# Kernel optimization log

Hardware: AMD Instinct MI355X
Metric: run time of the kernel (lower is better)

## Reference

```python
import math
import jax, jax.numpy as jnp
import numpy as np

B, S, D = 64, 729, 64  # S = (32*14//16 - 1)**2

def setup_inputs() -> dict:
    key = jax.random.key(0)
    kq, kk, kv, km = jax.random.split(key, 4)
    return {
        "query": jax.random.normal(kq, (B, S, D), dtype=jnp.float32),
        "key": jax.random.normal(kk, (B, S, D), dtype=jnp.float32),
        "value": jax.random.normal(kv, (B, S, D), dtype=jnp.float32),
        "mask": jax.random.randint(km, (B, S, S), 0, 2, dtype=jnp.int32),
    }

def reference(query, key, value, mask):
    dk = query.shape[-1]
    # [B,S,S] scores
    scores = jnp.einsum('bqd,bkd->bqk', query, key) / math.sqrt(dk)
    scores = jnp.where(mask == 0, jnp.float32(-1e9), scores)
    attention = jnp.tanh(scores)  # args.activation == 'tanh'
    # ignore_diag == 1: zero the diagonal of each [S,S] attention map
    eye = jnp.eye(attention.shape[-1], dtype=attention.dtype)
    attention = attention * (1.0 - eye)
    out = jnp.einsum('bqk,bkd->bqd', attention, value)
    return (out, attention)
```

## Files before the change

kernel.cpp:

```cpp
#include <hip/hip_runtime.h>

#define BATCH 64
#define SEQ 729
#define DIM 64
#define NT 12
#define STRB 72
#define MSTR 68
#define OSTR 68

typedef __attribute__((ext_vector_type(8))) short bf16x8;
typedef __attribute__((ext_vector_type(4))) float f32x4;
typedef int   i32x4a __attribute__((ext_vector_type(4), aligned(4)));
typedef float f32x4a __attribute__((ext_vector_type(4), aligned(4)));

__device__ __forceinline__ unsigned short f2bf(float f) {
    unsigned int u = __float_as_uint(f);
    u += 0x7fffu + ((u >> 16) & 1u);
    return (unsigned short)(u >> 16);
}

__device__ __forceinline__ unsigned long long pack4bf(float a, float b, float c, float d) {
    return (unsigned long long)f2bf(a)
         | ((unsigned long long)f2bf(b) << 16)
         | ((unsigned long long)f2bf(c) << 32)
         | ((unsigned long long)f2bf(d) << 48);
}

__device__ __forceinline__ float bf2f(unsigned int hi16) {
    return __uint_as_float(hi16 << 16);
}

__device__ __forceinline__ float fast_tanh(float x) {
    float e = __builtin_amdgcn_exp2f(x * 2.88539008177792681f);
    return 1.0f - 2.0f * __builtin_amdgcn_rcpf(e + 1.0f);
}

#define BAR() do { \
    asm volatile("s_waitcnt lgkmcnt(0)" ::: "memory"); \
    __builtin_amdgcn_s_barrier(); \
    __builtin_amdgcn_sched_barrier(0); \
} while (0)

__global__ __launch_bounds__(256, 3) void attn_kernel(
    const float* __restrict__ Qg, const float* __restrict__ Kg,
    const float* __restrict__ Vg, const int* __restrict__ Mg,
    float* __restrict__ Og, float* __restrict__ Ag)
{
    __shared__ __align__(16) unsigned char smem[50432];
    unsigned short* Ks0 = (unsigned short*)(smem);
    unsigned short* Vs0 = (unsigned short*)(smem + 9216);
    unsigned short* Ks1 = (unsigned short*)(smem + 18432);
    unsigned short* Vs1 = (unsigned short*)(smem + 27648);
    unsigned short* Ps  = (unsigned short*)(smem + 36864);
    unsigned char*  Mb8 = smem + 46080;
    float* Ostage = (float*)smem;

    const int tid = threadIdx.x;
    const int q0  = blockIdx.x * 64;
    const int b   = blockIdx.y;

    const float* Qb = Qg + (size_t)b * SEQ * DIM;
    const float* Kb = Kg + (size_t)b * SEQ * DIM;
    const float* Vb = Vg + (size_t)b * SEQ * DIM;
    const int*   Mb = Mg + (size_t)b * SEQ * SEQ;
    float* Ob = Og + (size_t)b * SEQ * DIM;
    float* Ab = Ag + (size_t)b * SEQ * SEQ;

    const int lane = tid & 63;
    const int quad = lane >> 4;
    const int l15  = lane & 15;
    const int qrow = (tid >> 6) * 16;

    const int rr = tid >> 4;
    const int cc = (tid & 15) * 4;
    const int vd0 = (tid & 15) * 4;
    const int vk0 = (tid >> 4) * 4;
    const int prow = qrow + (lane >> 4);
    const int pcol = (lane & 15) * 4;

    float4 kr[4], vr[4];
    i32x4a mr[4];

    auto load_k = [&](int k0n) {
        #pragma unroll
        for (int i = 0; i < 4; ++i) {
            int gk = k0n + rr + 16 * i;
            kr[i] = (gk < SEQ) ? *(const float4*)(Kb + gk * DIM + cc)
                               : float4{0, 0, 0, 0};
        }
    };
    auto load_v = [&](int k0n) {
        #pragma unroll
        for (int i = 0; i < 4; ++i) {
            int gk = k0n + vk0 + i;
            vr[i] = (gk < SEQ) ? *(const float4*)(Vb + gk * DIM + vd0)
                               : float4{0, 0, 0, 0};
        }
    };
    auto load_mask = [&](int k0n) {
        #pragma unroll
        for (int i = 0; i < 4; ++i) {
            int gq = q0 + prow + 4 * i;
            int gk = k0n + pcol;
            if (gq < SEQ && gk + 3 < SEQ) {
                mr[i] = *(const i32x4a*)(Mb + (size_t)gq * SEQ + gk);
            } else if (gq < SEQ) {
                i32x4a t;
                #pragma unroll
                for (int e = 0; e < 4; ++e)
                    t[e] = (gk + e < SEQ) ? Mb[(size_t)gq * SEQ + gk + e] : 0;
                mr[i] = t;
            } else {
                mr[i] = i32x4a{0, 0, 0, 0};
            }
        }
    };
    auto drain_mask = [&]() {
        #pragma unroll
        for (int i = 0; i < 4; ++i) {
            unsigned int mb = (unsigned)(mr[i][0] & 1)
                            | ((unsigned)(mr[i][1] & 1) << 8)
                            | ((unsigned)(mr[i][2] & 1) << 16)
                            | ((unsigned)(mr[i][3] & 1) << 24);
            *(unsigned int*)&Mb8[(prow + 4 * i) * MSTR + pcol] = mb;
        }
    };
    auto drain_k = [&](unsigned short* Kd) {
        #pragma unroll
        for (int i = 0; i < 4; ++i)
            *(unsigned long long*)&Kd[(rr + 16 * i) * STRB + cc] =
                pack4bf(kr[i].x, kr[i].y, kr[i].z, kr[i].w);
    };
    auto drain_v = [&](unsigned short* Vd) {
        #pragma unroll
        for (int j = 0; j < 4; ++j) {
            float v0 = j==0?vr[0].x:j==1?vr[0].y:j==2?vr[0].z:vr[0].w;
            float v1 = j==0?vr[1].x:j==1?vr[1].y:j==2?vr[1].z:vr[1].w;
            float v2 = j==0?vr[2].x:j==1?vr[2].y:j==2?vr[2].z:vr[2].w;
            float v3 = j==0?vr[3].x:j==1?vr[3].y:j==2?vr[3].z:vr[3].w;
            *(unsigned long long*)&Vd[(vd0 + j) * STRB + vk0] = pack4bf(v0, v1, v2, v3);
        }
    };

    load_k(0); load_v(0); load_mask(0);
    #pragma unroll
    for (int i = 0; i < 4; ++i) {
        int gq = q0 + rr + 16 * i;
        float4 x = (gq < SEQ) ? *(const float4*)(Qb + gq * DIM + cc)
                              : float4{0, 0, 0, 0};
        *(unsigned long long*)&Ps[(rr + 16 * i) * STRB + cc] = pack4bf(x.x, x.y, x.z, x.w);
    }
    BAR();

    const bf16x8 aq0 = *(const bf16x8*)&Ps[(qrow + l15) * STRB + quad * 8];
    const bf16x8 aq1 = *(const bf16x8*)&Ps[(qrow + l15) * STRB + 32 + quad * 8];

    drain_mask();
    drain_k(Ks0);
    drain_v(Vs0);
    load_k(64); load_v(64); load_mask(64);
    BAR();

    f32x4 oacc[4];
    #pragma unroll
    for (int dt = 0; dt < 4; ++dt) {
        oacc[dt][0]=0.f; oacc[dt][1]=0.f; oacc[dt][2]=0.f; oacc[dt][3]=0.f;
    }

    for (int t = 0; t < NT; ++t) {
        const int k0 = t * 64;
        const unsigned short* KsC = (t & 1) ? Ks1 : Ks0;
        const unsigned short* VsC = (t & 1) ? Vs1 : Vs0;
        unsigned short* KsN = (t & 1) ? Ks0 : Ks1;
        unsigned short* VsN = (t & 1) ? Vs0 : Vs1;

        if (t + 1 < NT) drain_k(KsN);
        if (t + 2 < NT) load_k(k0 + 128);

        f32x4 sacc[4];
        #pragma unroll
        for (int n = 0; n < 4; ++n) {
            bf16x8 bk0 = *(const bf16x8*)&KsC[(n * 16 + l15) * STRB + quad * 8];
            bf16x8 bk1 = *(const bf16x8*)&KsC[(n * 16 + l15) * STRB + 32 + quad * 8];
            f32x4 c; c[0]=0.f; c[1]=0.f; c[2]=0.f; c[3]=0.f;
            c = __builtin_amdgcn_mfma_f32_16x16x32_bf16(aq0, bk0, c, 0, 0, 0);
            c = __builtin_amdgcn_mfma_f32_16x16x32_bf16(aq1, bk1, c, 0, 0, 0);
            sacc[n] = c;
        }

        #pragma unroll
        for (int n = 0; n < 4; ++n) {
            int col = n * 16 + l15;
            int gk  = k0 + col;
            #pragma unroll
            for (int r = 0; r < 4; ++r) {
                int qloc = qrow + quad * 4 + r;
                int gq = q0 + qloc;
                int m = Mb8[qloc * MSTR + col];
                float sv = sacc[n][r] * 0.125f;
                float p = fast_tanh((m == 0) ? -1e9f : sv);
                if (gq == gk || gk >= SEQ) p = 0.0f;
                Ps[qloc * STRB + col] = f2bf(p);
            }
        }

        #pragma unroll
        for (int i = 0; i < 4; ++i) {
            int row = prow + 4 * i;
            int gq  = q0 + row;
            int gk  = k0 + pcol;
            unsigned long long w = *(const unsigned long long*)&Ps[row * STRB + pcol];
            f32x4 pv;
            pv[0] = bf2f((unsigned)(w      ) & 0xffffu);
            pv[1] = bf2f((unsigned)(w >> 16) & 0xffffu);
            pv[2] = bf2f((unsigned)(w >> 32) & 0xffffu);
            pv[3] = bf2f((unsigned)(w >> 48) & 0xffffu);
            if (gq < SEQ) {
                if (gk + 3 < SEQ) {
                    *(f32x4a*)(Ab + (size_t)gq * SEQ + gk) = pv;
                } else {
                    #pragma unroll
                    for (int e = 0; e < 4; ++e)
                        if (gk + e < SEQ) Ab[(size_t)gq * SEQ + gk + e] = pv[e];
                }
            }
        }

        const bf16x8 ap0 = *(const bf16x8*)&Ps[(qrow + l15) * STRB + quad * 8];
        const bf16x8 ap1 = *(const bf16x8*)&Ps[(qrow + l15) * STRB + 32 + quad * 8];
        #pragma unroll
        for (int dt = 0; dt < 4; ++dt) {
            bf16x8 bv0 = *(const bf16x8*)&VsC[(dt * 16 + l15) * STRB + quad * 8];
            bf16x8 bv1 = *(const bf16x8*)&VsC[(dt * 16 + l15) * STRB + 32 + quad * 8];
            oacc[dt] = __builtin_amdgcn_mfma_f32_16x16x32_bf16(ap0, bv0, oacc[dt], 0, 0, 0);
            oacc[dt] = __builtin_amdgcn_mfma_f32_16x16x32_bf16(ap1, bv1, oacc[dt], 0, 0, 0);
        }

        if (t + 1 < NT) {
            drain_mask();
            drain_v(VsN);
            if (t + 2 < NT) {
                load_v(k0 + 128); load_mask(k0 + 128);
            }
            BAR();
        }
    }

    BAR();
    #pragma unroll
    for (int dt = 0; dt < 4; ++dt)
        #pragma unroll
        for (int r = 0; r < 4; ++r)
            Ostage[(qrow + quad * 4 + r) * OSTR + dt * 16 + l15] = oacc[dt][r];
    #pragma unroll
    for (int i = 0; i < 4; ++i) {
        int row = prow + 4 * i;
        int gq  = q0 + row;
        f32x4 ov = *(const f32x4*)&Ostage[row * OSTR + pcol];
        if (gq < SEQ) *(f32x4*)(Ob + (size_t)gq * DIM + pcol) = ov;
    }
}

extern "C" void kernel_launch(void* const* d_in, const int* in_sizes, int n_in,
                              void* d_out, int out_size, void* d_ws, size_t ws_size,
                              hipStream_t stream) {
    const float* Q = (const float*)d_in[0];
    const float* K = (const float*)d_in[1];
    const float* V = (const float*)d_in[2];
    const int*   M = (const int*)d_in[3];
    float* Out  = (float*)d_out;
    float* Attn = Out + (size_t)BATCH * SEQ * DIM;
    dim3 grid(NT, BATCH);
    attn_kernel<<<grid, 256, 0, stream>>>(Q, K, V, M, Out, Attn);
}
```

Measured before the change: 323.2 us.

## Pre-pack int32 mask into per-row bitmasks in a separate kernel

Adds a pack_mask kernel that reads the int32 mask once and uses wave ballots to write 64-bit bitmask words per row into workspace. The attention kernel then loads a small packed tile of mask words into shared memory at start, instead of streaming int32 mask tiles through registers and LDS every iteration. This takes mask traffic and register pressure out of the main pipelined loop. In exchange it adds a second launch and an extra pass that still reads the full mask, plus a small workspace write and read.

```diff
diff --git a/kernel.cpp b/kernel.cpp
--- a/kernel.cpp
+++ b/kernel.cpp
@@ -5,12 +5,12 @@
 #define DIM 64
 #define NT 12
 #define STRB 72
-#define MSTR 68
 #define OSTR 68
+#define MWPR 12
+#define MPST 13
 
 typedef __attribute__((ext_vector_type(8))) short bf16x8;
 typedef __attribute__((ext_vector_type(4))) float f32x4;
-typedef int   i32x4a __attribute__((ext_vector_type(4), aligned(4)));
 typedef float f32x4a __attribute__((ext_vector_type(4), aligned(4)));
 
 __device__ __forceinline__ unsigned short f2bf(float f) {
@@ -41,18 +41,36 @@
     __builtin_amdgcn_sched_barrier(0); \
 } while (0)
 
+__global__ __launch_bounds__(256) void pack_mask(
+    const int* __restrict__ Mg, unsigned long long* __restrict__ W)
+{
+    const int lane  = threadIdx.x & 63;
+    const int wave  = (blockIdx.x * 256 + threadIdx.x) >> 6;
+    const int nwave = (gridDim.x * 256) >> 6;
+    for (int row = wave; row < BATCH * SEQ; row += nwave) {
+        const int* Mr = Mg + (size_t)row * SEQ;
+        #pragma unroll
+        for (int w = 0; w < MWPR; ++w) {
+            int col = w * 64 + lane;
+            int m = (col < SEQ) ? Mr[col] : 0;
+            unsigned long long bal = __ballot(m != 0);
+            if (lane == 0) W[(size_t)row * MWPR + w] = bal;
+        }
+    }
+}
+
 __global__ __launch_bounds__(256, 3) void attn_kernel(
     const float* __restrict__ Qg, const float* __restrict__ Kg,
-    const float* __restrict__ Vg, const int* __restrict__ Mg,
+    const float* __restrict__ Vg, const unsigned long long* __restrict__ Wg,
     float* __restrict__ Og, float* __restrict__ Ag)
 {
-    __shared__ __align__(16) unsigned char smem[50432];
+    __shared__ __align__(16) unsigned char smem[52736];
     unsigned short* Ks0 = (unsigned short*)(smem);
     unsigned short* Vs0 = (unsigned short*)(smem + 9216);
     unsigned short* Ks1 = (unsigned short*)(smem + 18432);
     unsigned short* Vs1 = (unsigned short*)(smem + 27648);
     unsigned short* Ps  = (unsigned short*)(smem + 36864);
-    unsigned char*  Mb8 = smem + 46080;
+    unsigned long long* Mpk = (unsigned long long*)(smem + 46080);
     float* Ostage = (float*)smem;
 
     const int tid = threadIdx.x;
@@ -62,9 +80,9 @@
     const float* Qb = Qg + (size_t)b * SEQ * DIM;
     const float* Kb = Kg + (size_t)b * SEQ * DIM;
     const float* Vb = Vg + (size_t)b * SEQ * DIM;
-    const int*   Mb = Mg + (size_t)b * SEQ * SEQ;
     float* Ob = Og + (size_t)b * SEQ * DIM;
     float* Ab = Ag + (size_t)b * SEQ * SEQ;
+    const unsigned long long* Wb = Wg + ((size_t)b * SEQ + q0) * MWPR;
 
     const int lane = tid & 63;
     const int quad = lane >> 4;
@@ -79,7 +97,6 @@
     const int pcol = (lane & 15) * 4;
 
     float4 kr[4], vr[4];
-    i32x4a mr[4];
 
     auto load_k = [&](int k0n) {
         #pragma unroll
@@ -95,34 +112,6 @@
             int gk = k0n + vk0 + i;
             vr[i] = (gk < SEQ) ? *(const float4*)(Vb + gk * DIM + vd0)
                                : float4{0, 0, 0, 0};
-        }
-    };
-    auto load_mask = [&](int k0n) {
-        #pragma unroll
-        for (int i = 0; i < 4; ++i) {
-            int gq = q0 + prow + 4 * i;
-            int gk = k0n + pcol;
-            if (gq < SEQ && gk + 3 < SEQ) {
-                mr[i] = *(const i32x4a*)(Mb + (size_t)gq * SEQ + gk);
-            } else if (gq < SEQ) {
-                i32x4a t;
-                #pragma unroll
-                for (int e = 0; e < 4; ++e)
-                    t[e] = (gk + e < SEQ) ? Mb[(size_t)gq * SEQ + gk + e] : 0;
-                mr[i] = t;
-            } else {
-                mr[i] = i32x4a{0, 0, 0, 0};
-            }
-        }
-    };
-    auto drain_mask = [&]() {
-        #pragma unroll
-        for (int i = 0; i < 4; ++i) {
-            unsigned int mb = (unsigned)(mr[i][0] & 1)
-                            | ((unsigned)(mr[i][1] & 1) << 8)
-                            | ((unsigned)(mr[i][2] & 1) << 16)
-                            | ((unsigned)(mr[i][3] & 1) << 24);
-            *(unsigned int*)&Mb8[(prow + 4 * i) * MSTR + pcol] = mb;
         }
     };
     auto drain_k = [&](unsigned short* Kd) {
@@ -142,7 +131,16 @@
         }
     };
 
-    load_k(0); load_v(0); load_mask(0);
+    load_k(0); load_v(0);
+
+    #pragma unroll
+    for (int i = 0; i < 3; ++i) {
+        int idx = tid + 256 * i;
+        int r = idx / MWPR, w = idx - r * MWPR;
+        unsigned long long word = (q0 + r < SEQ) ? Wb[idx] : 0ull;
+        Mpk[r * MPST + w] = word;
+    }
+
     #pragma unroll
     for (int i = 0; i < 4; ++i) {
         int gq = q0 + rr + 16 * i;
@@ -155,10 +153,9 @@
     const bf16x8 aq0 = *(const bf16x8*)&Ps[(qrow + l15) * STRB + quad * 8];
     const bf16x8 aq1 = *(const bf16x8*)&Ps[(qrow + l15) * STRB + 32 + quad * 8];
 
-    drain_mask();
     drain_k(Ks0);
     drain_v(Vs0);
-    load_k(64); load_v(64); load_mask(64);
+    load_k(64); load_v(64);
     BAR();
 
     f32x4 oacc[4];
@@ -188,6 +185,11 @@
             sacc[n] = c;
         }
 
+        unsigned long long mw[4];
+        #pragma unroll
+        for (int r = 0; r < 4; ++r)
+            mw[r] = Mpk[(qrow + quad * 4 + r) * MPST + t];
+
         #pragma unroll
         for (int n = 0; n < 4; ++n) {
             int col = n * 16 + l15;
@@ -196,9 +198,9 @@
             for (int r = 0; r < 4; ++r) {
                 int qloc = qrow + quad * 4 + r;
                 int gq = q0 + qloc;
-                int m = Mb8[qloc * MSTR + col];
+                bool unmasked = (mw[r] >> col) & 1ull;
                 float sv = sacc[n][r] * 0.125f;
-                float p = fast_tanh((m == 0) ? -1e9f : sv);
+                float p = fast_tanh(unmasked ? sv : -1e9f);
                 if (gq == gk || gk >= SEQ) p = 0.0f;
                 Ps[qloc * STRB + col] = f2bf(p);
             }
@@ -237,11 +239,8 @@
         }
 
         if (t + 1 < NT) {
-            drain_mask();
             drain_v(VsN);
-            if (t + 2 < NT) {
-                load_v(k0 + 128); load_mask(k0 + 128);
-            }
+            if (t + 2 < NT) load_v(k0 + 128);
             BAR();
         }
     }
@@ -270,6 +269,9 @@
     const int*   M = (const int*)d_in[3];
     float* Out  = (float*)d_out;
     float* Attn = Out + (size_t)BATCH * SEQ * DIM;
+    unsigned long long* Wk = (unsigned long long*)d_ws;
+
+    pack_mask<<<dim3(2048), 256, 0, stream>>>(M, Wk);
     dim3 grid(NT, BATCH);
-    attn_kernel<<<grid, 256, 0, stream>>>(Q, K, V, M, Out, Attn);
-}
+    attn_kernel<<<grid, 256, 0, stream>>>(Q, K, V, Wk, Out, Attn);
+}
```

Result: no change. 327.5 us (+1.3%).
